# Kernel tuning notes

Measured on AMD Instinct MI355X. Metric: run time of the kernel, lower is better.

The kernel has to match this reference:

```python
import jax, jax.numpy as jnp
import numpy as np

VOCAB, D, B, T = 32000, 1024, 4, 2048

def setup_inputs() -> dict:
    key = jax.random.key(0)
    ks = jax.random.split(key, 7)
    std = 0.01  # model initializes all weights with std=0.01
    return {
        "x": jax.random.randint(ks[0], (B, T), 0, VOCAB),
        "emb_w": jax.random.normal(ks[1], (VOCAB, D), jnp.float32) * std,
        "wq": jax.random.normal(ks[2], (D, D), jnp.float32) * std,
        "wk": jax.random.normal(ks[3], (D, D), jnp.float32) * std,
        "wv": jax.random.normal(ks[4], (D, D), jnp.float32) * std,
        "wo": jax.random.normal(ks[5], (D, D), jnp.float32) * std,
        "wout": jax.random.normal(ks[6], (VOCAB, D), jnp.float32) * std,
    }

def fhe_act(x):
    # polynomial activation: 0.1*x^2 + 0.1*x
    return x * x * 0.1 + x * 0.1

def reference(x, emb_w, wq, wk, wv, wo, wout):
    h = emb_w[x] * 0.01                                 # [B,T,D]
    q = (h @ wq.T) * 0.01                               # [B,T,D]
    k = (h @ wk.T) * 0.01                               # [B,T,D]
    v = (h @ wv.T) * 0.1                                # [B,T,D]
    attn = jnp.einsum('btd,bsd->bts', q, k) * 0.01      # [B,T,T] full (no causal mask)
    attn = fhe_act(attn)
    out = jnp.einsum('bts,bsd->btd', attn, v) * 0.01    # [B,T,D]
    out = (out @ wo.T) * 0.1                            # [B,T,D]
    logits = out @ wout.T                               # [B,T,VOCAB]
    return logits
```

## Files before the change

kernel.cpp:

```cpp
#include <hip/hip_runtime.h>


typedef __bf16 bf16_t;
typedef __bf16 bf16x8 __attribute__((ext_vector_type(8)));
typedef __bf16 bf16x4 __attribute__((ext_vector_type(4)));
typedef float  f32x4  __attribute__((ext_vector_type(4)));

#define VOCAB 32000
#define DIM   1024
#define BATCH 4
#define SEQ   2048
#define BT    (BATCH*SEQ)

__device__ __forceinline__ void gload_lds16(const void* g, void* l) {
    __builtin_amdgcn_global_load_lds(
        (const __attribute__((address_space(1))) void*)g,
        (__attribute__((address_space(3))) void*)l,
        16, 0, 0);
}

__global__ void cast_f32_to_bf16(const float* __restrict__ in, bf16_t* __restrict__ out, int n4) {
    int i = blockIdx.x * blockDim.x + threadIdx.x;
    if (i < n4) {
        float4 v = ((const float4*)in)[i];
        bf16x4 o;
        o.x = (bf16_t)v.x; o.y = (bf16_t)v.y; o.z = (bf16_t)v.z; o.w = (bf16_t)v.w;
        ((bf16x4*)out)[i] = o;
    }
}

__global__ void embed_gather(const int* __restrict__ x, const float* __restrict__ emb,
                             bf16_t* __restrict__ h) {
    const int tok = blockIdx.x;
    const int row = x[tok];
    const float4* src = (const float4*)(emb + (long)row * DIM);
    bf16x4* dst = (bf16x4*)(h + (long)tok * DIM);
    int j = threadIdx.x;
    float4 v = src[j];
    bf16x4 o;
    o.x = (bf16_t)(v.x * 0.01f); o.y = (bf16_t)(v.y * 0.01f);
    o.z = (bf16_t)(v.z * 0.01f); o.w = (bf16_t)(v.w * 0.01f);
    dst[j] = o;
}

#define BAR() asm volatile("s_barrier" ::: "memory")
#define LGKM0() do { asm volatile("s_waitcnt lgkmcnt(0)" ::: "memory");               \
                     __builtin_amdgcn_sched_barrier(0); } while (0)

template<int ACT, int SWZ, typename CT>
__global__ __launch_bounds__(512, 2) void gemm_bt_256(
    const bf16_t* __restrict__ A, const bf16_t* __restrict__ B, CT* __restrict__ C,
    int N, int K, int lda, int ldb, long sA, long sB, long sC, float scale)
{
    __shared__ __align__(16) char smem[131072];
    char* const sm = smem;

    const int bz = blockIdx.z;
    A += (long)bz * sA;  B += (long)bz * sB;  C += (long)bz * sC;

    const int lin = blockIdx.x;
    int tm, tn;
    if (SWZ == 0) { const int xcd = lin & 7, jj = lin >> 3; tm = xcd * 4 + (jj & 3); tn = jj >> 2; }
    else          { tm = lin & 7; tn = lin >> 3; }
    const long trow0 = (long)tm * 256, tcol0 = (long)tn * 256;

    const int tid  = threadIdx.x;
    const int lane = tid & 63;
    const int wave = tid >> 6;
    const int wm = wave >> 2;
    const int wn = wave & 3;
    const int lr = lane & 15;
    const int ko2 = (lane >> 4) * 16;
    const int rbase = lr * 64 + (ko2 ^ (((lr >> 1) & 3) << 4));

    const int o0 = tid * 16, o1 = 8192 + tid * 16;
    int sr0, sc0, sr1, sc1;
    {
        int ol = o0 ^ (((o0 >> 7) & 3) << 4);
        sr0 = ((ol >> 10) >> 1) * 16 + ((ol >> 6) & 15);
        sc0 = ((ol >> 10) & 1) * 32 + ((ol & 63) >> 1);
        ol = o1 ^ (((o1 >> 7) & 3) << 4);
        sr1 = ((ol >> 10) >> 1) * 16 + ((ol >> 6) & 15);
        sc1 = ((ol >> 10) & 1) * 32 + ((ol & 63) >> 1);
    }

    const bf16_t* Abase = A + trow0 * lda;
    const bf16_t* Bbase = B + tcol0 * ldb;

#define STAGE_HT(gbase, ld, kt, half, ldsh) do {                                      \
    gload_lds16((gbase) + (long)((half) * 128 + sr0) * (ld) + ((kt) * 64 + sc0), (ldsh) + o0); \
    gload_lds16((gbase) + (long)((half) * 128 + sr1) * (ld) + ((kt) * 64 + sc1), (ldsh) + o1); \
} while (0)

    f32x4 acc[8][4];
#pragma unroll
    for (int i = 0; i < 8; ++i)
#pragma unroll
        for (int j = 0; j < 4; ++j)
            acc[i][j] = (f32x4){0.f, 0.f, 0.f, 0.f};

#define PHASE_LO(ks, ...) do {                                                        \
    bf16x8 af_[4];                                                                    \
    af_[0] = *(const bf16x8*)(ldsA + ((wm * 4 + 0) * 2 + (ks)) * 1024 + rbase);       \
    _Pragma("unroll")                                                                 \
    for (int c_ = 0; c_ < 4; ++c_)                                                    \
        bv_[c_] = *(const bf16x8*)(ldsB + (c_ >> 1) * 16384 +                         \
                      ((wn * 2 + (c_ & 1)) * 2 + (ks)) * 1024 + rbase);               \
    _Pragma("unroll")                                                                 \
    for (int i_ = 1; i_ < 4; ++i_)                                                    \
        af_[i_] = *(const bf16x8*)(ldsA +                                             \
                      ((wm * 4 + i_) * 2 + (ks)) * 1024 + rbase);                     \
    __VA_ARGS__;                                                                      \
    BAR();                                                                            \
    LGKM0();                                                                          \
    __builtin_amdgcn_s_setprio(1);                                                    \
    _Pragma("unroll")                                                                 \
    for (int i_ = 0; i_ < 4; ++i_)                                                    \
        _Pragma("unroll")                                                             \
        for (int c_ = 0; c_ < 4; ++c_)                                                \
            acc[i_][c_] = __builtin_amdgcn_mfma_f32_16x16x32_bf16(                    \
                af_[i_], bv_[c_], acc[i_][c_], 0, 0, 0);                              \
    __builtin_amdgcn_s_setprio(0);                                                    \
    __builtin_amdgcn_sched_barrier(0);                                                \
    BAR();                                                                            \
} while (0)

#define PHASE_HI(ks, ...) do {                                                        \
    bf16x8 af_[4];                                                                    \
    _Pragma("unroll")                                                                 \
    for (int i_ = 0; i_ < 4; ++i_)                                                    \
        af_[i_] = *(const bf16x8*)(ldsA + 16384 +                                     \
                      ((wm * 4 + i_) * 2 + (ks)) * 1024 + rbase);                     \
    __VA_ARGS__;                                                                      \
    BAR();                                                                            \
    LGKM0();                                                                          \
    __builtin_amdgcn_s_setprio(1);                                                    \
    _Pragma("unroll")                                                                 \
    for (int i_ = 0; i_ < 4; ++i_)                                                    \
        _Pragma("unroll")                                                             \
        for (int c_ = 0; c_ < 4; ++c_)                                                \
            acc[4 + i_][c_] = __builtin_amdgcn_mfma_f32_16x16x32_bf16(                \
                af_[i_], bv_[c_], acc[4 + i_][c_], 0, 0, 0);                          \
    __builtin_amdgcn_s_setprio(0);                                                    \
    __builtin_amdgcn_sched_barrier(0);                                                \
} while (0)

    {
        char* a0 = sm;
        char* b0 = sm + 32768;
        char* a1 = sm + 65536;
        char* b1 = sm + 65536 + 32768;
        STAGE_HT(Abase, lda, 0, 0, a0);
        STAGE_HT(Bbase, ldb, 0, 0, b0);
        STAGE_HT(Abase, lda, 0, 1, a0 + 16384);
        STAGE_HT(Bbase, ldb, 0, 1, b0 + 16384);
        STAGE_HT(Abase, lda, 1, 0, a1);
        STAGE_HT(Bbase, ldb, 1, 0, b1);
        asm volatile("s_waitcnt vmcnt(4)" ::: "memory");
        BAR();
    }

    const int NT = K / 64;
    for (int t = 0; t < NT; ++t) {
        const int buf = t & 1;
        char* ldsA  = sm + buf * 65536;
        char* ldsB  = ldsA + 32768;
        char* ldsAn = sm + (buf ^ 1) * 65536;
        char* ldsBn = ldsAn + 32768;
        bf16x8 bv_[4];

        PHASE_LO(0,
              if (t + 1 < NT) {
                  STAGE_HT(Abase, lda, t + 1, 1, ldsAn + 16384);
                  STAGE_HT(Bbase, ldb, t + 1, 1, ldsBn + 16384);
              });
        PHASE_HI(0, );
        BAR();
        PHASE_LO(1, );
        PHASE_HI(1,
              if (t + 2 < NT) {
                  STAGE_HT(Abase, lda, t + 2, 0, ldsA);
                  STAGE_HT(Bbase, ldb, t + 2, 0, ldsB);
              });
        if (t + 2 < NT) { asm volatile("s_waitcnt vmcnt(4)" ::: "memory"); }
        else            { asm volatile("s_waitcnt vmcnt(0)" ::: "memory"); }
        BAR();
    }

    const int erow = (lane >> 4) * 4;
    const int ecol = lane & 15;
#pragma unroll
    for (int a = 0; a < 8; ++a)
#pragma unroll
        for (int c = 0; c < 4; ++c)
#pragma unroll
            for (int r = 0; r < 4; ++r) {
                long row = trow0 + (a >> 2) * 128 + wm * 64 + (a & 3) * 16 + erow + r;
                long col = tcol0 + (c >> 1) * 128 + wn * 32 + (c & 1) * 16 + ecol;
                float s = acc[a][c][r] * scale;
                if (ACT) s = s * s * 0.1f + s * 0.1f;
                C[row * N + col] = (CT)s;
            }
#undef PHASE_LO
#undef PHASE_HI
#undef STAGE_HT
}

template<int ACT, int SWZ, typename CT>
__global__ __launch_bounds__(512, 4) void gemm_bt_256x128(
    const bf16_t* __restrict__ A, const bf16_t* __restrict__ B, CT* __restrict__ C,
    int N, int K, long sA, long sB, long sC, float scale)
{
    __shared__ __align__(16) char smem[2 * 24576];
    char* const sm = smem;

    const int bz = blockIdx.z;
    A += (long)bz * sA;  B += (long)bz * sB;  C += (long)bz * sC;

    const int lin = blockIdx.x;
    int tm, tn;
    if      (SWZ == 0) { const int xcd = lin & 7, jj = lin >> 3; tm = xcd * 4 + (jj & 3); tn = jj >> 2; }
    else if (SWZ == 1) { tm = lin & 7; tn = lin >> 3; }
    else               { tm = lin & 3; tn = lin >> 2; }
    const long trow0 = (long)tm * 256, tcol0 = (long)tn * 128;

    const int tid  = threadIdx.x;
    const int lane = tid & 63;
    const int wave = tid >> 6;
    const int wm = wave >> 1;
    const int wn = wave & 1;
    const int lr = lane & 15;
    const int ko2 = (lane >> 4) * 16;
    const int rbase = lr * 64 + (ko2 ^ (((lr >> 1) & 3) << 4));

    const int o0 = tid * 16;
    const int ol = o0 ^ (((o0 >> 7) & 3) << 4);
    const int sr = (ol >> 10) * 16 + ((ol >> 6) & 15);
    const int sc = (ol & 63) >> 1;

    const bf16_t* Abase = A + trow0 * K;
    const bf16_t* Bbase = B + tcol0 * K;

#define STAGE_A(kt, bufp) do {                                                        \
    gload_lds16(Abase + (long)sr * K         + ((kt) * 32 + sc), (bufp) + o0);        \
    gload_lds16(Abase + (long)(128 + sr) * K + ((kt) * 32 + sc), (bufp) + 8192 + o0); \
} while (0)
#define STAGE_B(kt, bufp) do {                                                        \
    gload_lds16(Bbase + (long)sr * K + ((kt) * 32 + sc), (bufp) + 16384 + o0);        \
} while (0)

    f32x4 acc[4][4];
#pragma unroll
    for (int i = 0; i < 4; ++i)
#pragma unroll
        for (int j = 0; j < 4; ++j)
            acc[i][j] = (f32x4){0.f, 0.f, 0.f, 0.f};

    STAGE_A(0, sm);
    STAGE_B(0, sm);
    STAGE_A(1, sm + 24576);
    asm volatile("s_waitcnt vmcnt(2)" ::: "memory");
    BAR();

    const int NT = K / 32;
    for (int t = 0; t < NT; ++t) {
        char* cur = sm + (t & 1) * 24576;
        char* idl = sm + ((t & 1) ^ 1) * 24576;

        bf16x8 af_[4], bvA[2], bvB[2];
        af_[0] = *(const bf16x8*)(cur + (wm * 4 + 0) * 1024 + rbase);
        bvA[0] = *(const bf16x8*)(cur + 16384 + (wn * 2 + 0) * 1024 + rbase);
        bvA[1] = *(const bf16x8*)(cur + 16384 + (wn * 2 + 1) * 1024 + rbase);
#pragma unroll
        for (int i = 1; i < 4; ++i)
            af_[i] = *(const bf16x8*)(cur + (wm * 4 + i) * 1024 + rbase);
        if (t + 1 < NT) STAGE_B(t + 1, idl);
        BAR();
        LGKM0();
        __builtin_amdgcn_s_setprio(1);
#pragma unroll
        for (int i = 0; i < 4; ++i) {
            acc[i][0] = __builtin_amdgcn_mfma_f32_16x16x32_bf16(af_[i], bvA[0], acc[i][0], 0, 0, 0);
            acc[i][1] = __builtin_amdgcn_mfma_f32_16x16x32_bf16(af_[i], bvA[1], acc[i][1], 0, 0, 0);
        }
        __builtin_amdgcn_s_setprio(0);
        __builtin_amdgcn_sched_barrier(0);
        BAR();

        bvB[0] = *(const bf16x8*)(cur + 16384 + (4 + wn * 2 + 0) * 1024 + rbase);
        bvB[1] = *(const bf16x8*)(cur + 16384 + (4 + wn * 2 + 1) * 1024 + rbase);
        if (t + 2 < NT) STAGE_A(t + 2, cur);
        BAR();
        LGKM0();
        __builtin_amdgcn_s_setprio(1);
#pragma unroll
        for (int i = 0; i < 4; ++i) {
            acc[i][2] = __builtin_amdgcn_mfma_f32_16x16x32_bf16(af_[i], bvB[0], acc[i][2], 0, 0, 0);
            acc[i][3] = __builtin_amdgcn_mfma_f32_16x16x32_bf16(af_[i], bvB[1], acc[i][3], 0, 0, 0);
        }
        __builtin_amdgcn_s_setprio(0);
        __builtin_amdgcn_sched_barrier(0);
        if (t + 2 < NT) { asm volatile("s_waitcnt vmcnt(2)" ::: "memory"); }
        else            { asm volatile("s_waitcnt vmcnt(0)" ::: "memory"); }
        BAR();
    }

    const int erow = (lane >> 4) * 4;
    const int ecol = lane & 15;
#pragma unroll
    for (int i = 0; i < 4; ++i)
#pragma unroll
        for (int j = 0; j < 4; ++j)
#pragma unroll
            for (int r = 0; r < 4; ++r) {
                long row = trow0 + wm * 64 + i * 16 + erow + r;
                long col = tcol0 + (j >> 1) * 64 + wn * 32 + (j & 1) * 16 + ecol;
                float s = acc[i][j][r] * scale;
                if (ACT) s = s * s * 0.1f + s * 0.1f;
                C[row * N + col] = (CT)s;
            }
#undef STAGE_A
#undef STAGE_B
}

extern "C" void kernel_launch(void* const* d_in, const int* in_sizes, int n_in,
                              void* d_out, int out_size, void* d_ws, size_t ws_size,
                              hipStream_t stream) {
    const int*   x    = (const int*)d_in[0];
    const float* emb  = (const float*)d_in[1];
    const float* wq   = (const float*)d_in[2];
    const float* wk   = (const float*)d_in[3];
    const float* wv   = (const float*)d_in[4];
    const float* wo   = (const float*)d_in[5];
    const float* wout = (const float*)d_in[6];
    float* logits = (float*)d_out;

    char* ws = (char*)d_ws;
    size_t off = 0;
    auto alloc = [&](size_t bytes) {
        char* p = ws + off;
        off += (bytes + 255) & ~(size_t)255;
        return p;
    };
    bf16_t* hb    = (bf16_t*)alloc((size_t)BT * DIM * 2);
    bf16_t* qkb   = (bf16_t*)alloc((size_t)BT * 2 * DIM * 2);
    bf16_t* vtb   = (bf16_t*)alloc((size_t)BATCH * DIM * SEQ * 2);
    bf16_t* attnb = (bf16_t*)alloc((size_t)BATCH * SEQ * SEQ * 2);
    bf16_t* o1b   = (bf16_t*)alloc((size_t)BT * DIM * 2);
    bf16_t* o2b   = (bf16_t*)alloc((size_t)BT * DIM * 2);
    bf16_t* wqkb  = (bf16_t*)alloc((size_t)2 * DIM * DIM * 2);
    bf16_t* wvb   = (bf16_t*)alloc((size_t)DIM * DIM * 2);
    bf16_t* wob   = (bf16_t*)alloc((size_t)DIM * DIM * 2);
    bf16_t* woutb = (bf16_t*)alloc((size_t)VOCAB * DIM * 2);

    {
        int n4 = DIM * DIM / 4;
        cast_f32_to_bf16<<<n4 / 256, 256, 0, stream>>>(wq, wqkb, n4);
        cast_f32_to_bf16<<<n4 / 256, 256, 0, stream>>>(wk, wqkb + (size_t)DIM * DIM, n4);
        cast_f32_to_bf16<<<n4 / 256, 256, 0, stream>>>(wv, wvb, n4);
        cast_f32_to_bf16<<<n4 / 256, 256, 0, stream>>>(wo, wob, n4);
        int n4o = VOCAB * DIM / 4;
        cast_f32_to_bf16<<<n4o / 256, 256, 0, stream>>>(wout, woutb, n4o);
    }

    embed_gather<<<BT, 256, 0, stream>>>(x, emb, hb);

    gemm_bt_256x128<0, 0, bf16_t><<<dim3((BT / 256) * (2 * DIM / 128), 1, 1), 512, 0, stream>>>(
        hb, wqkb, qkb, 2 * DIM, DIM, 0, 0, 0, 0.01f);

    gemm_bt_256x128<0, 2, bf16_t><<<dim3(64, 1, BATCH), 512, 0, stream>>>(
        wvb, hb, vtb, SEQ, DIM, 0, (long)SEQ * DIM, (long)DIM * SEQ, 0.1f);

    gemm_bt_256<1, 1, bf16_t><<<dim3(64, 1, BATCH), 512, 0, stream>>>(
        qkb, qkb + DIM, attnb, SEQ, DIM, 2 * DIM, 2 * DIM,
        (long)SEQ * 2 * DIM, (long)SEQ * 2 * DIM, (long)SEQ * SEQ, 0.01f);

    gemm_bt_256x128<0, 1, bf16_t><<<dim3(64, 1, BATCH), 512, 0, stream>>>(
        attnb, vtb, o1b, DIM, SEQ,
        (long)SEQ * SEQ, (long)DIM * SEQ, (long)SEQ * DIM, 0.01f);

    gemm_bt_256x128<0, 0, bf16_t><<<dim3((BT / 256) * (DIM / 128), 1, 1), 512, 0, stream>>>(
        o1b, wob, o2b, DIM, DIM, 0, 0, 0, 0.1f);

    gemm_bt_256x128<0, 0, float><<<dim3((BT / 256) * (VOCAB / 128), 1, 1), 512, 0, stream>>>(
        o2b, woutb, logits, VOCAB, DIM, 0, 0, 0, 1.0f);
}
```

Baseline: 891.2 us.

## Triple-buffer LDS in 256x128 GEMM and drop redundant barriers in phase macros

The 256x128 GEMM kernel moves from a double-buffered, two-half iteration with staggered A/B staging to a three-slot LDS ring. Each iteration now reads all fragments, issues the loads for tile t+2, and runs all 16 MFMAs after one barrier. Separately, the 256x256 kernel's phase macros lose the barrier and LDS-count wait before their MFMA blocks, cutting synchronization. In exchange, LDS per block grows to 72KB, which likely reduces the number of resident blocks per CU. Removing the barriers relies on compiler-inserted waits and on the remaining barriers still ordering LDS reuse correctly.

```diff
diff --git a/kernel.cpp b/kernel.cpp
--- a/kernel.cpp
+++ b/kernel.cpp
@@ -111,8 +111,6 @@
         af_[i_] = *(const bf16x8*)(ldsA +                                             \
                       ((wm * 4 + i_) * 2 + (ks)) * 1024 + rbase);                     \
     __VA_ARGS__;                                                                      \
-    BAR();                                                                            \
-    LGKM0();                                                                          \
     __builtin_amdgcn_s_setprio(1);                                                    \
     _Pragma("unroll")                                                                 \
     for (int i_ = 0; i_ < 4; ++i_)                                                    \
@@ -132,8 +130,6 @@
         af_[i_] = *(const bf16x8*)(ldsA + 16384 +                                     \
                       ((wm * 4 + i_) * 2 + (ks)) * 1024 + rbase);                     \
     __VA_ARGS__;                                                                      \
-    BAR();                                                                            \
-    LGKM0();                                                                          \
     __builtin_amdgcn_s_setprio(1);                                                    \
     _Pragma("unroll")                                                                 \
     for (int i_ = 0; i_ < 4; ++i_)                                                    \
@@ -211,7 +207,7 @@
     const bf16_t* __restrict__ A, const bf16_t* __restrict__ B, CT* __restrict__ C,
     int N, int K, long sA, long sB, long sC, float scale)
 {
-    __shared__ __align__(16) char smem[2 * 24576];
+    __shared__ __align__(16) char smem[3 * 24576];
     char* const sm = smem;
 
     const int bz = blockIdx.z;
@@ -256,53 +252,43 @@
         for (int j = 0; j < 4; ++j)
             acc[i][j] = (f32x4){0.f, 0.f, 0.f, 0.f};
 
-    STAGE_A(0, sm);
-    STAGE_B(0, sm);
-    STAGE_A(1, sm + 24576);
-    asm volatile("s_waitcnt vmcnt(2)" ::: "memory");
+    STAGE_A(0, sm);             STAGE_B(0, sm);
+    STAGE_A(1, sm + 24576);     STAGE_B(1, sm + 24576);
+    asm volatile("s_waitcnt vmcnt(3)" ::: "memory");
     BAR();
 
     const int NT = K / 32;
+    int bi = 0;
     for (int t = 0; t < NT; ++t) {
-        char* cur = sm + (t & 1) * 24576;
-        char* idl = sm + ((t & 1) ^ 1) * 24576;
-
-        bf16x8 af_[4], bvA[2], bvB[2];
+        char* cur = sm + bi * 24576;
+        const int bn = (bi + 2 >= 3) ? bi - 1 : bi + 2;
+        char* nxt = sm + bn * 24576;
+
+        bf16x8 af_[4], bv_[4];
         af_[0] = *(const bf16x8*)(cur + (wm * 4 + 0) * 1024 + rbase);
-        bvA[0] = *(const bf16x8*)(cur + 16384 + (wn * 2 + 0) * 1024 + rbase);
-        bvA[1] = *(const bf16x8*)(cur + 16384 + (wn * 2 + 1) * 1024 + rbase);
+        bv_[0] = *(const bf16x8*)(cur + 16384 + (wn * 2 + 0) * 1024 + rbase);
+        bv_[1] = *(const bf16x8*)(cur + 16384 + (wn * 2 + 1) * 1024 + rbase);
 #pragma unroll
         for (int i = 1; i < 4; ++i)
             af_[i] = *(const bf16x8*)(cur + (wm * 4 + i) * 1024 + rbase);
-        if (t + 1 < NT) STAGE_B(t + 1, idl);
+        bv_[2] = *(const bf16x8*)(cur + 16384 + (4 + wn * 2 + 0) * 1024 + rbase);
+        bv_[3] = *(const bf16x8*)(cur + 16384 + (4 + wn * 2 + 1) * 1024 + rbase);
+        if (t + 2 < NT) { STAGE_A(t + 2, nxt); STAGE_B(t + 2, nxt); }
         BAR();
         LGKM0();
         __builtin_amdgcn_s_setprio(1);
 #pragma unroll
-        for (int i = 0; i < 4; ++i) {
-            acc[i][0] = __builtin_amdgcn_mfma_f32_16x16x32_bf16(af_[i], bvA[0], acc[i][0], 0, 0, 0);
-            acc[i][1] = __builtin_amdgcn_mfma_f32_16x16x32_bf16(af_[i], bvA[1], acc[i][1], 0, 0, 0);
-        }
+        for (int i = 0; i < 4; ++i)
+#pragma unroll
+            for (int j = 0; j < 4; ++j)
+                acc[i][j] = __builtin_amdgcn_mfma_f32_16x16x32_bf16(
+                    af_[i], bv_[j], acc[i][j], 0, 0, 0);
         __builtin_amdgcn_s_setprio(0);
         __builtin_amdgcn_sched_barrier(0);
-        BAR();
-
-        bvB[0] = *(const bf16x8*)(cur + 16384 + (4 + wn * 2 + 0) * 1024 + rbase);
-        bvB[1] = *(const bf16x8*)(cur + 16384 + (4 + wn * 2 + 1) * 1024 + rbase);
-        if (t + 2 < NT) STAGE_A(t + 2, cur);
-        BAR();
-        LGKM0();
-        __builtin_amdgcn_s_setprio(1);
-#pragma unroll
-        for (int i = 0; i < 4; ++i) {
-            acc[i][2] = __builtin_amdgcn_mfma_f32_16x16x32_bf16(af_[i], bvB[0], acc[i][2], 0, 0, 0);
-            acc[i][3] = __builtin_amdgcn_mfma_f32_16x16x32_bf16(af_[i], bvB[1], acc[i][3], 0, 0, 0);
-        }
-        __builtin_amdgcn_s_setprio(0);
-        __builtin_amdgcn_sched_barrier(0);
-        if (t + 2 < NT) { asm volatile("s_waitcnt vmcnt(2)" ::: "memory"); }
+        if (t + 2 < NT) { asm volatile("s_waitcnt vmcnt(3)" ::: "memory"); }
         else            { asm volatile("s_waitcnt vmcnt(0)" ::: "memory"); }
         BAR();
+        bi = (bi == 2) ? 0 : bi + 1;
     }
 
     const int erow = (lane >> 4) * 4;
```

New measurement: 881.5 us. Within noise of the previous version (-1.1%).
